# Kernel tuning notes

Hardware: AMD Instinct MI355X
Metric: run time of the kernel (lower is better)

Reference implementation:

```python
import jax, jax.numpy as jnp
import numpy as np

EPS_BN = 1e-5
EPS_LN = 1e-5


def _conv1d_same(x, w, b):
    # x: [B,C,L], w: [O,C,K], 'same' padding, stride 1
    y = jax.lax.conv_general_dilated(x, w, (1,), 'SAME',
                                     dimension_numbers=('NCH', 'OIH', 'NCH'))
    return y + b[None, :, None]


def _bn_eval(x, g, b, m, v):
    # BatchNorm1d in eval mode over channel dim of [B,C,L]
    return (x - m[None, :, None]) * jax.lax.rsqrt(v[None, :, None] + EPS_BN) \
        * g[None, :, None] + b[None, :, None]


def _layernorm_ch(x, g, b):
    # x: [B,H,L]; normalize over channel dim H (torch does transpose->LN->transpose)
    xt = jnp.swapaxes(x, -1, -2)  # [B,L,H]
    mu = xt.mean(-1, keepdims=True)
    var = ((xt - mu) ** 2).mean(-1, keepdims=True)
    xt = (xt - mu) * jax.lax.rsqrt(var + EPS_LN) * g + b
    return jnp.swapaxes(xt, -1, -2)


def _s4d_layer(u, log_dt, A_re_log, A_im, C_re, C_im, D, out_w, out_b):
    # S4D (diagonal SSM) block: FFT long convolution + D skip + GELU + GLU output linear
    B, H, L = u.shape
    dt = jnp.exp(log_dt)                       # [H]
    A = -jnp.exp(A_re_log) + 1j * A_im         # [H,N] diagonal state matrix
    C = C_re + 1j * C_im                       # [H,N]
    dtA = A * dt[:, None]                      # [H,N]
    coef = C * (jnp.exp(dtA) - 1.0) / A        # ZOH discretization (S4D-Lin)
    # Vandermonde kernel: K[h,l] = 2 Re sum_n coef[h,n] * exp(dtA[h,n]*l)
    vand = jnp.exp(dtA[:, :, None] * jnp.arange(L, dtype=jnp.float32))  # [H,N,L]
    K = 2.0 * jnp.real(jnp.einsum('hn,hnl->hl', coef, vand))            # [H,L]
    # non-circular convolution via length-2L FFT
    n = 2 * L
    yf = jnp.fft.rfft(u, n=n) * jnp.fft.rfft(K, n=n)[None]
    y = jnp.fft.irfft(yf, n=n)[..., :L]
    y = y + D[None, :, None] * u               # skip connection
    y = jax.nn.gelu(y)
    # position-wise output linear (Conv1d kernel 1, H -> 2H) + GLU over channels
    z = jnp.einsum('oh,bhl->bol', out_w, y) + out_b[None, :, None]
    z1, z2 = jnp.split(z, 2, axis=1)
    return z1 * jax.nn.sigmoid(z2)


def setup_inputs() -> dict:
    key = jax.random.key(0)
    ks = jax.random.split(key, 32)
    B, L = 16, 4096
    chans = [1, 64, 128, 256]
    ksz = [7, 5, 3]
    H, N, NL, DOUT = 256, 64, 4, 10
    d = {}
    d['x'] = jax.random.normal(ks[0], (B, 1, L), dtype=jnp.float32)
    for i in range(3):
        ci, co, k = chans[i], chans[i + 1], ksz[i]
        scale = 1.0 / np.sqrt(ci * k)
        d[f'conv_w{i}'] = jax.random.normal(ks[1 + i], (co, ci, k), dtype=jnp.float32) * scale
        d[f'conv_b{i}'] = jnp.zeros((co,), dtype=jnp.float32)
        d[f'bn_g{i}'] = jnp.ones((co,), dtype=jnp.float32)
        d[f'bn_b{i}'] = jnp.zeros((co,), dtype=jnp.float32)
        d[f'bn_m{i}'] = jax.random.normal(ks[4 + i], (co,), dtype=jnp.float32) * 0.1
        d[f'bn_v{i}'] = jnp.ones((co,), dtype=jnp.float32)
    # S4D params, stacked over layers
    u01 = jax.random.uniform(ks[10], (NL, H), dtype=jnp.float32)
    d['log_dt'] = np.log(0.001) + u01 * (np.log(0.1) - np.log(0.001))
    d['A_re_log'] = jnp.full((NL, H, N), np.log(0.5), dtype=jnp.float32)
    d['A_im'] = jnp.broadcast_to(np.pi * jnp.arange(N, dtype=jnp.float32), (NL, H, N)).copy()
    d['C_re'] = jax.random.normal(ks[11], (NL, H, N), dtype=jnp.float32) * (0.5 ** 0.5)
    d['C_im'] = jax.random.normal(ks[12], (NL, H, N), dtype=jnp.float32) * (0.5 ** 0.5)
    d['D'] = jax.random.normal(ks[13], (NL, H), dtype=jnp.float32)
    d['out_w'] = jax.random.normal(ks[14], (NL, 2 * H, H), dtype=jnp.float32) / np.sqrt(H)
    d['out_b'] = jnp.zeros((NL, 2 * H), dtype=jnp.float32)
    d['ln_g'] = jnp.ones((NL, H), dtype=jnp.float32)
    d['ln_b'] = jnp.zeros((NL, H), dtype=jnp.float32)
    d['dec_w'] = jax.random.normal(ks[15], (DOUT, H), dtype=jnp.float32) / np.sqrt(H)
    d['dec_b'] = jnp.zeros((DOUT,), dtype=jnp.float32)
    return d


def reference(x,
              conv_w0, conv_b0, bn_g0, bn_b0, bn_m0, bn_v0,
              conv_w1, conv_b1, bn_g1, bn_b1, bn_m1, bn_v1,
              conv_w2, conv_b2, bn_g2, bn_b2, bn_m2, bn_v2,
              log_dt, A_re_log, A_im, C_re, C_im, D, out_w, out_b,
              ln_g, ln_b, dec_w, dec_b):
    # Encoder: (conv -> BN(eval) -> ReLU) x 3   (pool is never registered in original)
    convs = [(conv_w0, conv_b0, bn_g0, bn_b0, bn_m0, bn_v0),
             (conv_w1, conv_b1, bn_g1, bn_b1, bn_m1, bn_v1),
             (conv_w2, conv_b2, bn_g2, bn_b2, bn_m2, bn_v2)]
    for (cw, cb, g, b, m, v) in convs:
        x = jax.nn.relu(_bn_eval(_conv1d_same(x, cw, cb), g, b, m, v))
    # stacked S4 layers with residual + post-LayerNorm (prenorm=False), dropout=identity (eval)
    n_layers = log_dt.shape[0]
    for l in range(n_layers):
        z = _s4d_layer(x, log_dt[l], A_re_log[l], A_im[l],
                       C_re[l], C_im[l], D[l], out_w[l], out_b[l])
        x = z + x
        x = _layernorm_ch(x, ln_g[l], ln_b[l])
    # mean-pool over time, decode
    x = jnp.swapaxes(x, -1, -2).mean(axis=1)   # [B,H]
    return x @ dec_w.T + dec_b
```

## Files before the change

### kernel.cpp

```cpp
#include <hip/hip_runtime.h>
#include <cstdint>
#include <cstddef>

#define L_SEQ 4096
#define H_DIM 256
#define N_MODES 64
#define BATCH 16
#define QCH 128
#define NCHUNK 32
#define LPAD (L_SEQ + 8)

typedef __attribute__((ext_vector_type(8))) short short8v;
typedef __attribute__((ext_vector_type(16))) float f32x16;

#define MFMA32(a, b, c) __builtin_amdgcn_mfma_f32_32x32x16_bf16((a), (b), (c), 0, 0, 0)

__device__ __forceinline__ unsigned short f2bf(float f) {
    unsigned u = __float_as_uint(f);
    u = u + 0x7fff + ((u >> 16) & 1);
    return (unsigned short)(u >> 16);
}
__device__ __forceinline__ float bf2f(unsigned short h) {
    return __uint_as_float(((unsigned)h) << 16);
}
__device__ __forceinline__ float fast_gelu(float y) {
    float t = fmaf(0.044715f * y * y, y, y);
    return y / (1.f + __expf(-1.5957691f * t));
}
__device__ __forceinline__ float fast_sigmoid_mul(float z1, float z2) {
    return z1 / (1.f + __expf(-z2));
}

__device__ __forceinline__ int bpos(int k, int col) {
    return ((col >> 5) * 8 + (k >> 4)) * 512 + ((col & 31) + 32 * ((k >> 3) & 1)) * 8 + (k & 7);
}
__device__ __forceinline__ void whi(unsigned short* M, int k, int col, float v) {
    M[bpos(k, col)] = f2bf(v);
}

__global__ __launch_bounds__(256) void mats_gen(
    const float* __restrict__ log_dt, const float* __restrict__ A_re_log,
    const float* __restrict__ A_im, const float* __restrict__ C_re,
    const float* __restrict__ C_im, const float* __restrict__ Dv, int layer,
    unsigned short* __restrict__ Vpk, unsigned short* __restrict__ Epk,
    unsigned short* __restrict__ Tpk, float* __restrict__ wqbuf)
{
    __shared__ float Kl[4][128];
    const int wv = threadIdx.x >> 6, n = threadIdx.x & 63;
    const int h = blockIdx.x * 4 + wv;
    const int idx = (layer * H_DIM + h) * N_MODES + n;
    float dt = expf(log_dt[layer * H_DIM + h]);
    float Ar = -expf(A_re_log[idx]);
    float Ai = A_im[idx];
    float dr = Ar * dt, di = Ai * dt;
    float er = expf(dr);
    float wr = er * cosf(di), wi = er * sinf(di);
    float nr = wr - 1.f, ni = wi;
    float Cr = C_re[idx], Ci = C_im[idx];
    float pr_ = Cr * nr - Ci * ni;
    float pi_ = Cr * ni + Ci * nr;
    float inv = 1.f / (Ar * Ar + Ai * Ai);
    float c2r = 2.f * (pr_ * Ar + pi_ * Ai) * inv;
    float c2i = 2.f * (pi_ * Ar - pr_ * Ai) * inv;
    float Dh = Dv[layer * H_DIM + h];
    unsigned short* Vh = Vpk + h * 32768;
    unsigned short* Eh = Epk + h * 32768;
    float pr = 1.f, pi = 0.f;
    for (int d = 0; d <= QCH; ++d) {
        float qr = c2r * pr - c2i * pi;
        float qi = c2r * pi + c2i * pr;
        if (d <= QCH - 1) {
            int t = QCH - 1 - d;
            whi(Vh, t, 2 * n, pr);
            whi(Vh, t, 2 * n + 1, pi);
            float s = qr;
            #pragma unroll
            for (int st = 1; st < 64; st <<= 1) s += __shfl_xor(s, st);
            if (n == 0) Kl[wv][d] = s + (d == 0 ? Dh : 0.f);
        }
        if (d >= 1) {
            int t = d - 1;
            whi(Eh, 2 * n, t, qr);
            whi(Eh, 2 * n + 1, t, -qi);
        }
        if (d == QCH) {
            wqbuf[(h * 64 + n) * 2 + 0] = pr;
            wqbuf[(h * 64 + n) * 2 + 1] = pi;
        }
        float npr = pr * wr - pi * wi;
        float npi = pr * wi + pi * wr;
        pr = npr; pi = npi;
    }
    __syncthreads();
    unsigned short* Th = Tpk + h * 32768;
    const float* Kh = Kl[wv];
    for (int g = 0; g < 32; ++g) {
        int nt = g >> 3, ks = g & 7;
        int col = nt * 32 + (n & 31);
        int k0 = ks * 16 + (n >> 5) * 8;
        union { unsigned short s[8]; uint4 v; } hi;
        #pragma unroll
        for (int j = 0; j < 8; ++j) {
            int d = col - (k0 + j);
            hi.s[j] = f2bf((d >= 0) ? Kh[d] : 0.f);
        }
        *(uint4*)(Th + (nt * 8 + ks) * 512 + n * 8) = hi.v;
    }
}

template<int CI, int K, int CO>
__global__ __launch_bounds__(256) void pack_conv(
    const float* __restrict__ wg, const float* __restrict__ g,
    const float* __restrict__ v, const float* __restrict__ cb,
    const float* __restrict__ m, const float* __restrict__ bb,
    unsigned short* __restrict__ Wc, float* __restrict__ Bs)
{
    constexpr int NT = CO / 32, KS = CI / 16;
    int t = blockIdx.x * 256 + threadIdx.x;
    if (t < CO) Bs[t] = (cb[t] - m[t]) * g[t] * rsqrtf(v[t] + 1e-5f) + bb[t];
    if (t >= K * NT * KS * 64) return;
    int lane = t & 63;
    int rest = t >> 6;
    int ks = rest % KS;
    int nt = (rest / KS) % NT;
    int k = rest / (KS * NT);
    int co = nt * 32 + (lane & 31);
    int ci0 = ks * 16 + (lane >> 5) * 8;
    float s = g[co] * rsqrtf(v[co] + 1e-5f);
    union { unsigned short s_[8]; uint4 v_; } hi, lo;
    #pragma unroll
    for (int j = 0; j < 8; ++j) {
        float f = wg[((size_t)co * CI + ci0 + j) * K + k] * s;
        hi.s_[j] = f2bf(f);
        lo.s_[j] = f2bf(f - bf2f(hi.s_[j]));
    }
    size_t base = ((size_t)(k * NT + nt) * KS + ks) * 512 + lane * 8;
    *(uint4*)(Wc + base) = hi.v_;
    *(uint4*)(Wc + base + (size_t)K * NT * KS * 512) = lo.v_;
}

template<int CI, int K>
__global__ __launch_bounds__(256) void conv_bn_relu_f(
    const float* __restrict__ in, float* __restrict__ out,
    const float* __restrict__ wg, const float* __restrict__ cb,
    const float* __restrict__ g, const float* __restrict__ bb,
    const float* __restrict__ m, const float* __restrict__ v, int CO)
{
    const int wv = threadIdx.x >> 6, lane = threadIdx.x & 63;
    const int b = blockIdx.z;
    const int co0 = __builtin_amdgcn_readfirstlane(blockIdx.y * 32 + wv * 8);
    const int l = blockIdx.x * 256 + lane * 4;
    const int OFF = K / 2;
    float acc[8][4] = {};
    const float* inb = in + (size_t)b * CI * L_SEQ;
    for (int ci = 0; ci < CI; ++ci) {
        const float* row = inb + (size_t)ci * L_SEQ;
        float win[12];
        #pragma unroll
        for (int d = 0; d < 12; ++d) {
            int li = l - 4 + d;
            win[d] = (li >= 0 && li < L_SEQ) ? row[li] : 0.f;
        }
        #pragma unroll
        for (int cc = 0; cc < 8; ++cc) {
            #pragma unroll
            for (int k = 0; k < K; ++k) {
                float wk = wg[((size_t)(co0 + cc) * CI + ci) * K + k];
                #pragma unroll
                for (int j = 0; j < 4; ++j)
                    acc[cc][j] = fmaf(win[4 + j + k - OFF], wk, acc[cc][j]);
            }
        }
    }
    #pragma unroll
    for (int cc = 0; cc < 8; ++cc) {
        int co = co0 + cc;
        float s = g[co] * rsqrtf(v[co] + 1e-5f);
        float sh = (cb[co] - m[co]) * s + bb[co];
        float* orow = out + ((size_t)b * CO + co) * LPAD + 4;
        float4 o4;
        o4.x = fmaxf(fmaf(acc[cc][0], s, sh), 0.f);
        o4.y = fmaxf(fmaf(acc[cc][1], s, sh), 0.f);
        o4.z = fmaxf(fmaf(acc[cc][2], s, sh), 0.f);
        o4.w = fmaxf(fmaf(acc[cc][3], s, sh), 0.f);
        *(float4*)(orow + l) = o4;
        if (blockIdx.x == 0 && lane == 0)
            *(float4*)(orow - 4) = make_float4(0.f, 0.f, 0.f, 0.f);
        if (blockIdx.x == gridDim.x - 1 && lane == 63)
            *(float4*)(orow + L_SEQ) = make_float4(0.f, 0.f, 0.f, 0.f);
    }
}

template<int CI, int K, int CO, bool POUT, bool OBF>
__global__ __launch_bounds__(256) void conv_mfma(
    const float* __restrict__ in, void* __restrict__ outv,
    const unsigned short* __restrict__ Wc, const float* __restrict__ Bs)
{
    constexpr int NT = CO / 32, KS = CI / 16, OBS = NT / 4, OFF = K / 2;
    constexpr int PLSZ = K * NT * KS * 512;
    __shared__ __align__(16) unsigned short A0[40 * CI];
    __shared__ __align__(16) unsigned short A1[40 * CI];
    __shared__ float vt[32][CO + 4];
    const int b = blockIdx.y, l0 = blockIdx.x * 32;
    const int wv = threadIdx.x >> 6, lane = threadIdx.x & 63;
    const float* inb = in + (size_t)b * CI * LPAD + l0;
    for (int e = threadIdx.x; e < CI * 10; e += 256) {
        int ci = e / 10, f4 = e - ci * 10;
        float4 q = *(const float4*)(inb + (size_t)ci * LPAD + f4 * 4);
        #pragma unroll
        for (int j = 0; j < 4; ++j) {
            int row = f4 * 4 + j;
            int bo = ((row * CI + ci) * 2) ^ ((row & 7) << 4);
            float f = (&q.x)[j];
            unsigned short h = f2bf(f);
            *(unsigned short*)((char*)A0 + bo) = h;
            *(unsigned short*)((char*)A1 + bo) = f2bf(f - bf2f(h));
        }
    }
    __syncthreads();
    f32x16 acc0 = {}, acc1 = {};
    #pragma unroll
    for (int k = 0; k < K; ++k) {
        #pragma unroll
        for (int ks = 0; ks < KS; ++ks) {
            int row = (lane & 31) + 4 + k - OFF;
            int abyte = ((row * CI + ks * 16 + (lane >> 5) * 8) * 2) ^ ((row & 7) << 4);
            short8v ah = *(const short8v*)((const char*)A0 + abyte);
            short8v al = *(const short8v*)((const char*)A1 + abyte);
            {
                const unsigned short* wb = Wc + ((size_t)(k * NT + wv * OBS) * KS + ks) * 512 + lane * 8;
                short8v bh = *(const short8v*)wb;
                short8v bl = *(const short8v*)(wb + PLSZ);
                acc0 = MFMA32(ah, bh, acc0);
                acc0 = MFMA32(ah, bl, acc0);
                acc0 = MFMA32(al, bh, acc0);
            }
            if constexpr (OBS == 2) {
                const unsigned short* wb = Wc + ((size_t)(k * NT + wv * OBS + 1) * KS + ks) * 512 + lane * 8;
                short8v bh = *(const short8v*)wb;
                short8v bl = *(const short8v*)(wb + PLSZ);
                acc1 = MFMA32(ah, bh, acc1);
                acc1 = MFMA32(ah, bl, acc1);
                acc1 = MFMA32(al, bh, acc1);
            }
        }
    }
    {
        int co = (wv * OBS) * 32 + (lane & 31);
        float bs = Bs[co];
        #pragma unroll
        for (int r = 0; r < 16; ++r) {
            int lr = (r & 3) + 8 * (r >> 2) + 4 * (lane >> 5);
            vt[lr][co] = fmaxf(acc0[r] + bs, 0.f);
        }
        if constexpr (OBS == 2) {
            int co1 = co + 32;
            float bs1 = Bs[co1];
            #pragma unroll
            for (int r = 0; r < 16; ++r) {
                int lr = (r & 3) + 8 * (r >> 2) + 4 * (lane >> 5);
                vt[lr][co1] = fmaxf(acc1[r] + bs1, 0.f);
            }
        }
    }
    __syncthreads();
    if constexpr (CO == 256) {
        if constexpr (OBF) {
            unsigned short* orow = (unsigned short*)outv
                + ((size_t)b * CO + threadIdx.x) * L_SEQ + l0;
            #pragma unroll
            for (int u8 = 0; u8 < 4; ++u8) {
                union { unsigned short s[8]; uint4 v; } pk;
                #pragma unroll
                for (int j = 0; j < 8; ++j)
                    pk.s[j] = f2bf(vt[u8 * 8 + j][threadIdx.x]);
                *(uint4*)(orow + u8 * 8) = pk.v;
            }
        } else {
            float* orow = (float*)outv + ((size_t)b * CO + threadIdx.x) * L_SEQ + l0;
            #pragma unroll
            for (int u4 = 0; u4 < 8; ++u4) {
                float4 o;
                o.x = vt[u4 * 4 + 0][threadIdx.x];
                o.y = vt[u4 * 4 + 1][threadIdx.x];
                o.z = vt[u4 * 4 + 2][threadIdx.x];
                o.w = vt[u4 * 4 + 3][threadIdx.x];
                *(float4*)(orow + u4 * 4) = o;
            }
        }
    } else {
        float* out = (float*)outv;
        int co = threadIdx.x & 127, lh = threadIdx.x >> 7;
        float* rowb = out + ((size_t)b * CO + co) * LPAD;
        float* orow = rowb + 4 + l0 + lh * 16;
        #pragma unroll
        for (int u4 = 0; u4 < 4; ++u4) {
            float4 o;
            o.x = vt[lh * 16 + u4 * 4 + 0][co];
            o.y = vt[lh * 16 + u4 * 4 + 1][co];
            o.z = vt[lh * 16 + u4 * 4 + 2][co];
            o.w = vt[lh * 16 + u4 * 4 + 3][co];
            *(float4*)(orow + u4 * 4) = o;
        }
        if (blockIdx.x == 0 && lh == 0)
            *(float4*)(rowb) = make_float4(0.f, 0.f, 0.f, 0.f);
        if (blockIdx.x == gridDim.x - 1 && lh == 1)
            *(float4*)(rowb + 4 + L_SEQ) = make_float4(0.f, 0.f, 0.f, 0.f);
    }
}

__global__ __launch_bounds__(256) void s4d_fused(
    const unsigned short* __restrict__ u,
    const unsigned short* __restrict__ Vpk,
    const unsigned short* __restrict__ Epk,
    const unsigned short* __restrict__ Tpk,
    const float* __restrict__ wqbuf,
    unsigned short* __restrict__ ybf)
{
    __shared__ __align__(16) unsigned short Sb[4][4096];
    const int h = blockIdx.x;
    const int wv = threadIdx.x >> 6, lane = threadIdx.x & 63;
    const int b = blockIdx.y * 4 + wv;
    const unsigned short* urow = u + ((size_t)b * H_DIM + h) * L_SEQ;
    const int c = lane & 31;
    const int khalf = (lane >> 5) * 8;
    char* Sw = (char*)Sb[wv];

    short8v uh[8];
    #pragma unroll
    for (int ks = 0; ks < 8; ++ks)
        uh[ks] = *(const short8v*)(urow + c * 128 + ks * 16 + khalf);

    f32x16 acc0 = {}, acc1 = {}, acc2 = {}, acc3 = {};
    {
        const unsigned short* Vh = Vpk + h * 32768;
        #pragma unroll
        for (int ks = 0; ks < 8; ++ks) {
            const unsigned short* vb = Vh + ks * 512 + lane * 8;
            short8v b0h = *(const short8v*)(vb);
            short8v b1h = *(const short8v*)(vb + 4096);
            short8v b2h = *(const short8v*)(vb + 8192);
            short8v b3h = *(const short8v*)(vb + 12288);
            acc0 = MFMA32(uh[ks], b0h, acc0);
            acc1 = MFMA32(uh[ks], b1h, acc1);
            acc2 = MFMA32(uh[ks], b2h, acc2);
            acc3 = MFMA32(uh[ks], b3h, acc3);
        }
    }
    #pragma unroll
    for (int nt = 0; nt < 4; ++nt) {
        const f32x16& a = nt == 0 ? acc0 : nt == 1 ? acc1 : nt == 2 ? acc2 : acc3;
        int col = nt * 32 + (lane & 31);
        #pragma unroll
        for (int r = 0; r < 16; ++r) {
            int cc = (r & 3) + 8 * (r >> 2) + 4 * (lane >> 5);
            int boff = (cc * 256 + col * 2) ^ ((cc & 15) << 4);
            *(unsigned short*)(Sw + boff) = f2bf(a[r]);
        }
    }
    __syncthreads();
    {
        const float2 wq = *(const float2*)(wqbuf + ((size_t)h * 64 + lane) * 2);
        float sr[NCHUNK], si[NCHUNK];
        #pragma unroll
        for (int cc = 0; cc < NCHUNK; ++cc) {
            int boff = (cc * 256 + lane * 4) ^ ((cc & 15) << 4);
            sr[cc] = bf2f(*(const unsigned short*)(Sw + boff));
            si[cc] = bf2f(*(const unsigned short*)(Sw + boff + 2));
        }
        float Pr = 0.f, Pi = 0.f;
        #pragma unroll
        for (int cc = 0; cc < NCHUNK; ++cc) {
            int boff = (cc * 256 + lane * 4) ^ ((cc & 15) << 4);
            *(unsigned short*)(Sw + boff) = f2bf(Pr);
            *(unsigned short*)(Sw + boff + 2) = f2bf(Pi);
            float npr = fmaf(wq.x, Pr, fmaf(-wq.y, Pi, sr[cc]));
            float npi = fmaf(wq.x, Pi, fmaf(wq.y, Pr, si[cc]));
            Pr = npr; Pi = npi;
        }
    }
    __syncthreads();
    acc0 = (f32x16){}; acc1 = (f32x16){}; acc2 = (f32x16){}; acc3 = (f32x16){};
    {
        const unsigned short* Eh = Epk + h * 32768;
        const unsigned short* Th = Tpk + h * 32768;
        const int swzc = (c & 15) << 4;
        #pragma unroll
        for (int ks = 0; ks < 8; ++ks) {
            int boff = (c * 256 + (ks * 16 + khalf) * 2) ^ swzc;
            short8v ah = *(const short8v*)(Sw + boff);
            const unsigned short* eb = Eh + ks * 512 + lane * 8;
            const unsigned short* tb = Th + ks * 512 + lane * 8;
            short8v e0 = *(const short8v*)(eb);
            short8v e1 = *(const short8v*)(eb + 4096);
            short8v e2 = *(const short8v*)(eb + 8192);
            short8v e3 = *(const short8v*)(eb + 12288);
            short8v t0 = *(const short8v*)(tb);
            short8v t1 = *(const short8v*)(tb + 4096);
            short8v t2 = *(const short8v*)(tb + 8192);
            short8v t3 = *(const short8v*)(tb + 12288);
            acc0 = MFMA32(ah, e0, acc0);
            acc1 = MFMA32(ah, e1, acc1);
            acc2 = MFMA32(ah, e2, acc2);
            acc3 = MFMA32(ah, e3, acc3);
            acc0 = MFMA32(uh[ks], t0, acc0);
            acc1 = MFMA32(uh[ks], t1, acc1);
            acc2 = MFMA32(uh[ks], t2, acc2);
            acc3 = MFMA32(uh[ks], t3, acc3);
        }
    }
    unsigned short* yrow = ybf + ((size_t)b * H_DIM + h) * L_SEQ;
    #pragma unroll
    for (int nt = 0; nt < 4; ++nt) {
        const f32x16& a = nt == 0 ? acc0 : nt == 1 ? acc1 : nt == 2 ? acc2 : acc3;
        int t = nt * 32 + (lane & 31);
        #pragma unroll
        for (int r = 0; r < 16; ++r) {
            int cc = (r & 3) + 8 * (r >> 2) + 4 * (lane >> 5);
            yrow[cc * QCH + t] = f2bf(fast_gelu(a[r]));
        }
    }
}

__global__ __launch_bounds__(256) void precompute_wpk(
    const float* __restrict__ W, unsigned short* __restrict__ Wpk)
{
    int t = blockIdx.x * 256 + threadIdx.x;
    if (t >= 4 * 16 * 16 * 64) return;
    int lane = t & 63;
    int kk = (t >> 6) & 15;
    int ob = (t >> 10) & 15;
    int layer = t >> 14;
    int o = ob * 32 + (lane & 31);
    int k0 = kk * 16 + (lane >> 5) * 8;
    const float* src = W + ((size_t)layer * 512 + o) * H_DIM + k0;
    union { unsigned short s[8]; uint4 v; } hi;
    #pragma unroll
    for (int j = 0; j < 8; ++j) hi.s[j] = f2bf(src[j]);
    size_t base = (size_t)layer * 262144 + ((size_t)((ob * 16 + kk) * 64 + lane) * 8);
    *(uint4*)(Wpk + base) = hi.v;
}

template<bool LAST>
__global__ __launch_bounds__(512) void linear_glu_ln(
    const unsigned short* __restrict__ ybf,
    const unsigned short* __restrict__ Wpk,
    const float* __restrict__ bias,
    const float* __restrict__ lg, const float* __restrict__ lb,
    unsigned short* __restrict__ xbf, float* __restrict__ meanb)
{
    __shared__ __align__(16) unsigned short Sm[2][8448];
    const int lane = threadIdx.x & 63;
    const int t = threadIdx.x >> 8;
    const int tid_t = threadIdx.x & 255;
    const int wv4 = (threadIdx.x >> 6) & 3;
    const int b = blockIdx.y;
    const int l0 = blockIdx.x * 64;
    const int lt0 = l0 + t * 32;
    unsigned short* Smt = Sm[t];

    {
        const unsigned short* ybase = ybf + (size_t)b * H_DIM * L_SEQ + lt0;
        #pragma unroll
        for (int p = 0; p < 4; ++p) {
            int e = tid_t + p * 256;
            int hh = e >> 2, c4 = e & 3;
            union { uint4 v; unsigned short s[8]; } qv;
            qv.v = *(const uint4*)(ybase + (size_t)hh * L_SEQ + c4 * 8);
            #pragma unroll
            for (int j = 0; j < 8; ++j) {
                int lloc = c4 * 8 + j;
                int byteoff = (lloc << 9) + hh * 2;
                byteoff ^= ((lloc & 15) << 4);
                *(unsigned short*)((char*)Smt + byteoff) = qv.s[j];
            }
        }
    }
    __syncthreads();

    const int ob0 = 2 * wv4, ob1 = 2 * wv4 + 1;
    const int r = lane & 31;
    const float4 g4 = *(const float4*)(lg + lane * 4);
    const float4 b4 = *(const float4*)(lb + lane * 4);
    float msum = 0.f;

    f32x16 acc0 = {}, acc1 = {}, acc2 = {}, acc3 = {};
    #pragma unroll 4
    for (int kk = 0; kk < 16; ++kk) {
        int abyte = (r << 9) | (kk * 32 + (lane >> 5) * 16);
        abyte ^= ((r & 15) << 4);
        short8v a = *(const short8v*)((char*)Smt + abyte);
        const unsigned short* w0 = Wpk + (((ob0 * 16 + kk) * 64 + lane) * 8);
        const unsigned short* w1 = Wpk + (((ob1 * 16 + kk) * 64 + lane) * 8);
        const unsigned short* w2 = Wpk + ((((ob0 + 8) * 16 + kk) * 64 + lane) * 8);
        const unsigned short* w3 = Wpk + ((((ob1 + 8) * 16 + kk) * 64 + lane) * 8);
        short8v h0 = *(const short8v*)w0;
        short8v h1 = *(const short8v*)w1;
        short8v h2 = *(const short8v*)w2;
        short8v h3 = *(const short8v*)w3;
        acc0 = MFMA32(a, h0, acc0);
        acc1 = MFMA32(a, h1, acc1);
        acc2 = MFMA32(a, h2, acc2);
        acc3 = MFMA32(a, h3, acc3);
    }
    __syncthreads();
    #pragma unroll
    for (int p = 0; p < 2; ++p) {
        const f32x16& z1v = p ? acc1 : acc0;
        const f32x16& z2v = p ? acc3 : acc2;
        int o = (p ? ob1 : ob0) * 32 + (lane & 31);
        float b1 = bias[o], b2 = bias[o + 256];
        #pragma unroll
        for (int rr = 0; rr < 16; ++rr) {
            int lloc = (rr & 3) + 8 * (rr >> 2) + 4 * (lane >> 5);
            Smt[lloc * 264 + o] = f2bf(fast_sigmoid_mul(z1v[rr] + b1, z2v[rr] + b2));
        }
    }
    __syncthreads();
    {
        const unsigned short* xr = xbf + ((size_t)b * H_DIM + tid_t) * L_SEQ + lt0;
        #pragma unroll
        for (int u8 = 0; u8 < 4; ++u8) {
            union { uint4 v; unsigned short s[8]; } q;
            q.v = *(const uint4*)(xr + u8 * 8);
            #pragma unroll
            for (int j = 0; j < 8; ++j) {
                int idx = (u8 * 8 + j) * 264 + tid_t;
                Smt[idx] = f2bf(bf2f(Smt[idx]) + bf2f(q.s[j]));
            }
        }
    }
    __syncthreads();
    #pragma unroll
    for (int rr = 0; rr < 8; ++rr) {
        int row = rr * 4 + wv4;
        ushort4 hv = *(const ushort4*)(Smt + row * 264 + lane * 4);
        float v0 = bf2f(hv.x), v1 = bf2f(hv.y), v2 = bf2f(hv.z), v3 = bf2f(hv.w);
        float s = v0 + v1 + v2 + v3;
        float sq = v0 * v0 + v1 * v1 + v2 * v2 + v3 * v3;
        #pragma unroll
        for (int st = 1; st < 64; st <<= 1) {
            s += __shfl_xor(s, st);
            sq += __shfl_xor(sq, st);
        }
        float mean = s * (1.f / H_DIM);
        float var = sq * (1.f / H_DIM) - mean * mean;
        float rstd = rsqrtf(var + 1e-5f);
        ushort4 ov;
        ov.x = f2bf((v0 - mean) * rstd * g4.x + b4.x);
        ov.y = f2bf((v1 - mean) * rstd * g4.y + b4.y);
        ov.z = f2bf((v2 - mean) * rstd * g4.z + b4.z);
        ov.w = f2bf((v3 - mean) * rstd * g4.w + b4.w);
        *(ushort4*)(Smt + row * 264 + lane * 4) = ov;
    }
    __syncthreads();
    {
        unsigned short* dst = xbf + ((size_t)b * H_DIM + tid_t) * L_SEQ + lt0;
        #pragma unroll
        for (int u8 = 0; u8 < 4; ++u8) {
            union { uint4 v; unsigned short s[8]; } pk;
            #pragma unroll
            for (int j = 0; j < 8; ++j) {
                pk.s[j] = Smt[(u8 * 8 + j) * 264 + tid_t];
                if constexpr (LAST) msum += bf2f(pk.s[j]);
            }
            *(uint4*)(dst + u8 * 8) = pk.v;
        }
    }
    if constexpr (LAST)
        atomicAdd(&meanb[b * H_DIM + tid_t], msum);
}

__global__ __launch_bounds__(256) void decode(
    const float* __restrict__ meanb, const float* __restrict__ dw,
    const float* __restrict__ db, float* __restrict__ out)
{
    int i = threadIdx.x;
    if (i >= BATCH * 10) return;
    int b = i / 10, d = i % 10;
    float s = db[d];
    for (int h = 0; h < H_DIM; ++h)
        s = fmaf(meanb[b * H_DIM + h] * (1.f / L_SEQ), dw[d * H_DIM + h], s);
    out[i] = s;
}

extern "C" void kernel_launch(void* const* d_in, const int* in_sizes, int n_in,
                              void* d_out, int out_size, void* d_ws, size_t ws_size,
                              hipStream_t stream)
{
    const float* x_in = (const float*)d_in[0];
    const float* cw[3] = {(const float*)d_in[1], (const float*)d_in[7],  (const float*)d_in[13]};
    const float* cb[3] = {(const float*)d_in[2], (const float*)d_in[8],  (const float*)d_in[14]};
    const float* bg[3] = {(const float*)d_in[3], (const float*)d_in[9],  (const float*)d_in[15]};
    const float* bb[3] = {(const float*)d_in[4], (const float*)d_in[10], (const float*)d_in[16]};
    const float* bm[3] = {(const float*)d_in[5], (const float*)d_in[11], (const float*)d_in[17]};
    const float* bv[3] = {(const float*)d_in[6], (const float*)d_in[12], (const float*)d_in[18]};
    const float* log_dt   = (const float*)d_in[19];
    const float* A_re_log = (const float*)d_in[20];
    const float* A_im     = (const float*)d_in[21];
    const float* C_re     = (const float*)d_in[22];
    const float* C_im     = (const float*)d_in[23];
    const float* Dv       = (const float*)d_in[24];
    const float* out_w    = (const float*)d_in[25];
    const float* out_b    = (const float*)d_in[26];
    const float* ln_g     = (const float*)d_in[27];
    const float* ln_b     = (const float*)d_in[28];
    const float* dec_w    = (const float*)d_in[29];
    const float* dec_b    = (const float*)d_in[30];

    const size_t PLANE = (size_t)BATCH * H_DIM * L_SEQ;
    float* ws = (float*)d_ws;
    unsigned short* xbf = (unsigned short*)ws;
    float* X   = ws + PLANE;
    unsigned short* ybf = (unsigned short*)(ws + 2 * PLANE);
    float* tail = ws + 2 * PLANE + PLANE / 2;
    unsigned short* Wpk = (unsigned short*)tail;
    float* Ktab  = tail + 524288;
    float* wqbuf = Ktab + 32768;
    float* meanb = wqbuf + 32768;
    unsigned short* Wc2 = (unsigned short*)(meanb + 4096);
    float* Bs2 = (float*)(Wc2 + 81920);
    unsigned short* Wc3 = (unsigned short*)(Bs2 + 128);
    float* Bs3 = (float*)(Wc3 + 196608);

    unsigned short* X_us = (unsigned short*)X;
    unsigned short* Vpk = X_us;
    unsigned short* Epk = X_us + 8388608;
    unsigned short* Tpk = X_us + 16777216;

    precompute_wpk<<<256, 256, 0, stream>>>(out_w, Wpk);
    pack_conv<64, 5, 128><<<20, 256, 0, stream>>>(cw[1], bg[1], bv[1], cb[1], bm[1], bb[1], Wc2, Bs2);
    pack_conv<128, 3, 256><<<48, 256, 0, stream>>>(cw[2], bg[2], bv[2], cb[2], bm[2], bb[2], Wc3, Bs3);
    hipMemsetAsync(meanb, 0, BATCH * H_DIM * sizeof(float), stream);

    float* c1p = X;
    float* c2p = X + (size_t)BATCH * 64 * LPAD;
    conv_bn_relu_f<1, 7><<<dim3(16, 2, 16), 256, 0, stream>>>(
        x_in, c1p, cw[0], cb[0], bg[0], bb[0], bm[0], bv[0], 64);
    conv_mfma<64, 5, 128, true, false><<<dim3(128, 16), 256, 0, stream>>>(c1p, c2p, Wc2, Bs2);
    conv_mfma<128, 3, 256, false, true><<<dim3(128, 16), 256, 0, stream>>>(c2p, xbf, Wc3, Bs3);

    for (int l = 0; l < 4; ++l) {
        mats_gen<<<64, 256, 0, stream>>>(log_dt, A_re_log, A_im, C_re, C_im, Dv, l,
                                         Vpk, Epk, Tpk, wqbuf);
        s4d_fused<<<dim3(256, 4), dim3(256), 0, stream>>>(xbf, Vpk, Epk, Tpk, wqbuf, ybf);
        if (l < 3)
            linear_glu_ln<false><<<dim3(64, 16), dim3(512), 0, stream>>>(
                ybf, Wpk + (size_t)l * 262144, out_b + l * 512,
                ln_g + l * H_DIM, ln_b + l * H_DIM, xbf, meanb);
        else
            linear_glu_ln<true><<<dim3(64, 16), dim3(512), 0, stream>>>(
                ybf, Wpk + (size_t)l * 262144, out_b + l * 512,
                ln_g + l * H_DIM, ln_b + l * H_DIM, xbf, meanb);
    }

    decode<<<dim3(1), 256, 0, stream>>>(meanb, dec_w, dec_b, (float*)d_out);
}
```

Baseline: 679.7 us.

## Alias conv epilogue buffer with bf16 staging and use wave-local LDS fences in s4d

In conv_mfma the epilogue staging buffer is now a raw byte array sized per output type, stored as bf16 when the output is bf16 and padded to CO+8, with an extra barrier before it is written. This shrinks LDS use and may raise occupancy. In s4d_fused two block-wide __syncthreads are replaced with a per-wave lgkmcnt wait plus sched_barrier. That relies on each wave only touching its own Sw slice and would race if any wave reads another wave's region.

```diff
diff --git a/kernel.cpp b/kernel.cpp
--- a/kernel.cpp
+++ b/kernel.cpp
@@ -22,6 +22,10 @@
 }
 __device__ __forceinline__ float bf2f(unsigned short h) {
     return __uint_as_float(((unsigned)h) << 16);
+}
+__device__ __forceinline__ void wave_lds_fence() {
+    asm volatile("s_waitcnt lgkmcnt(0)" ::: "memory");
+    __builtin_amdgcn_sched_barrier(0);
 }
 __device__ __forceinline__ float fast_gelu(float y) {
     float t = fmaf(0.044715f * y * y, y, y);
@@ -200,7 +204,7 @@
     constexpr int PLSZ = K * NT * KS * 512;
     __shared__ __align__(16) unsigned short A0[40 * CI];
     __shared__ __align__(16) unsigned short A1[40 * CI];
-    __shared__ float vt[32][CO + 4];
+    __shared__ __align__(16) char vtraw[32 * (CO + 8) * (OBF ? 2 : 4)];
     const int b = blockIdx.y, l0 = blockIdx.x * 32;
     const int wv = threadIdx.x >> 6, lane = threadIdx.x & 63;
     const float* inb = in + (size_t)b * CI * LPAD + l0;
@@ -245,13 +249,15 @@
             }
         }
     }
-    {
+    __syncthreads();
+    if constexpr (OBF) {
+        unsigned short* vtb = (unsigned short*)vtraw;
         int co = (wv * OBS) * 32 + (lane & 31);
         float bs = Bs[co];
         #pragma unroll
         for (int r = 0; r < 16; ++r) {
             int lr = (r & 3) + 8 * (r >> 2) + 4 * (lane >> 5);
-            vt[lr][co] = fmaxf(acc0[r] + bs, 0.f);
+            vtb[lr * (CO + 8) + co] = f2bf(fmaxf(acc0[r] + bs, 0.f));
         }
         if constexpr (OBS == 2) {
             int co1 = co + 32;
@@ -259,36 +265,41 @@
             #pragma unroll
             for (int r = 0; r < 16; ++r) {
                 int lr = (r & 3) + 8 * (r >> 2) + 4 * (lane >> 5);
-                vt[lr][co1] = fmaxf(acc1[r] + bs1, 0.f);
-            }
-        }
-    }
-    __syncthreads();
-    if constexpr (CO == 256) {
-        if constexpr (OBF) {
-            unsigned short* orow = (unsigned short*)outv
-                + ((size_t)b * CO + threadIdx.x) * L_SEQ + l0;
-            #pragma unroll
-            for (int u8 = 0; u8 < 4; ++u8) {
-                union { unsigned short s[8]; uint4 v; } pk;
+                vtb[lr * (CO + 8) + co1] = f2bf(fmaxf(acc1[r] + bs1, 0.f));
+            }
+        }
+        __syncthreads();
+        unsigned short* orow = (unsigned short*)outv
+            + ((size_t)b * CO + threadIdx.x) * L_SEQ + l0;
+        #pragma unroll
+        for (int u8 = 0; u8 < 4; ++u8) {
+            union { unsigned short s[8]; uint4 v; } pk;
+            #pragma unroll
+            for (int j = 0; j < 8; ++j)
+                pk.s[j] = vtb[(u8 * 8 + j) * (CO + 8) + threadIdx.x];
+            *(uint4*)(orow + u8 * 8) = pk.v;
+        }
+    } else {
+        float* vt = (float*)vtraw;
+        {
+            int co = (wv * OBS) * 32 + (lane & 31);
+            float bs = Bs[co];
+            #pragma unroll
+            for (int r = 0; r < 16; ++r) {
+                int lr = (r & 3) + 8 * (r >> 2) + 4 * (lane >> 5);
+                vt[lr * (CO + 8) + co] = fmaxf(acc0[r] + bs, 0.f);
+            }
+            if constexpr (OBS == 2) {
+                int co1 = co + 32;
+                float bs1 = Bs[co1];
                 #pragma unroll
-                for (int j = 0; j < 8; ++j)
-                    pk.s[j] = f2bf(vt[u8 * 8 + j][threadIdx.x]);
-                *(uint4*)(orow + u8 * 8) = pk.v;
-            }
-        } else {
-            float* orow = (float*)outv + ((size_t)b * CO + threadIdx.x) * L_SEQ + l0;
-            #pragma unroll
-            for (int u4 = 0; u4 < 8; ++u4) {
-                float4 o;
-                o.x = vt[u4 * 4 + 0][threadIdx.x];
-                o.y = vt[u4 * 4 + 1][threadIdx.x];
-                o.z = vt[u4 * 4 + 2][threadIdx.x];
-                o.w = vt[u4 * 4 + 3][threadIdx.x];
-                *(float4*)(orow + u4 * 4) = o;
-            }
-        }
-    } else {
+                for (int r = 0; r < 16; ++r) {
+                    int lr = (r & 3) + 8 * (r >> 2) + 4 * (lane >> 5);
+                    vt[lr * (CO + 8) + co1] = fmaxf(acc1[r] + bs1, 0.f);
+                }
+            }
+        }
+        __syncthreads();
         float* out = (float*)outv;
         int co = threadIdx.x & 127, lh = threadIdx.x >> 7;
         float* rowb = out + ((size_t)b * CO + co) * LPAD;
@@ -296,10 +307,10 @@
         #pragma unroll
         for (int u4 = 0; u4 < 4; ++u4) {
             float4 o;
-            o.x = vt[lh * 16 + u4 * 4 + 0][co];
-            o.y = vt[lh * 16 + u4 * 4 + 1][co];
-            o.z = vt[lh * 16 + u4 * 4 + 2][co];
-            o.w = vt[lh * 16 + u4 * 4 + 3][co];
+            o.x = vt[(lh * 16 + u4 * 4 + 0) * (CO + 8) + co];
+            o.y = vt[(lh * 16 + u4 * 4 + 1) * (CO + 8) + co];
+            o.z = vt[(lh * 16 + u4 * 4 + 2) * (CO + 8) + co];
+            o.w = vt[(lh * 16 + u4 * 4 + 3) * (CO + 8) + co];
             *(float4*)(orow + u4 * 4) = o;
         }
         if (blockIdx.x == 0 && lh == 0)
@@ -358,7 +369,7 @@
             *(unsigned short*)(Sw + boff) = f2bf(a[r]);
         }
     }
-    __syncthreads();
+    wave_lds_fence();
     {
         const float2 wq = *(const float2*)(wqbuf + ((size_t)h * 64 + lane) * 2);
         float sr[NCHUNK], si[NCHUNK];
@@ -379,7 +390,7 @@
             Pr = npr; Pi = npi;
         }
     }
-    __syncthreads();
+    wave_lds_fence();
     acc0 = (f32x16){}; acc1 = (f32x16){}; acc2 = (f32x16){}; acc3 = (f32x16){};
     {
         const unsigned short* Eh = Epk + h * 32768;
```

New measurement: 671.9 us. Within noise of the previous version (-1.2%).
